# Performance work log

Measured on AMD Instinct MI355X. Metric: run time of the kernel, lower is better.

The kernel has to match this reference:

```python
import jax, jax.numpy as jnp
import numpy as np

B, C, W, H = 16, 512, 64, 64
OUT, NH = 512, 8
HD = OUT // NH          # 64
K = 64                  # kernel_size == attended axis length (height)


def setup_inputs() -> dict:
    key = jax.random.key(0)
    k0, k1, k2, k3 = jax.random.split(key, 4)
    s = float(HD) ** -0.5
    return {
        "x": jax.random.normal(k0, (B, C, W, H), jnp.float32),
        "in_proj_weight": jax.random.normal(k1, (2 * OUT, C), jnp.float32) * s,
        "in_proj_bias": jnp.zeros((2 * OUT,), jnp.float32),
        "out_proj_w": jax.random.normal(k2, (OUT, OUT), jnp.float32) * s,
        "out_proj_b": jnp.zeros((OUT,), jnp.float32),
        "relative": jax.random.normal(k3, (2 * HD, 2 * K - 1), jnp.float32) * s,
    }


def reference(x, in_proj_weight, in_proj_bias, out_proj_w, out_proj_b, relative):
    b, c, w, h = x.shape
    hd2 = HD // 2
    # width=False, self-attention path: permute(0,3,2,1) then flat view
    xq = jnp.transpose(x, (0, 3, 2, 1)).reshape(b * w, h, c)
    qkv = xq @ in_proj_weight.T + in_proj_bias
    q, k, v = jnp.split(qkv, [OUT // 2, OUT], axis=2)

    # relative position embeddings gathered into [2*HD, K, K]
    rel_idx = jnp.arange(K)[:, None] - jnp.arange(K)[None, :] + (K - 1)  # key i, query j
    emb = relative[:, rel_idx]                                          # [2*HD, K, K]
    q_emb, k_emb, v_emb = jnp.split(emb, [hd2, HD], axis=0)

    # [bw, heads, ch, pos]
    q = q.reshape(b * w, h, NH, hd2).transpose(0, 2, 3, 1)
    k = k.reshape(b * w, h, NH, hd2).transpose(0, 2, 3, 1)
    v = v.reshape(b * w, h, NH, HD).transpose(0, 2, 3, 1)

    qr = jnp.einsum('bgci,cij->bgij', q, q_emb)
    kr = jnp.einsum('bgci,cij->bgij', k, k_emb).swapaxes(2, 3)
    qk = jnp.einsum('bgci,bgcj->bgij', q, k)
    sim = jax.nn.softmax(qk + qr + kr, axis=3)

    sv = jnp.einsum('bgij,bgcj->bgci', sim, v)     # [bw, NH, HD, h]
    sve = jnp.einsum('bgij,cij->bgci', sim, v_emb)  # [bw, NH, HD, h]
    out = (sv + sve).reshape(b * w, OUT, h).swapaxes(1, 2)  # [bw, h, OUT]
    out = out @ out_proj_w.T + out_proj_b
    # [b, w, h, OUT] -> transpose(2,3) -> permute(0,2,3,1) == transpose(0,3,2,1)
    out = out.reshape(b, w, h, OUT).transpose(0, 3, 2, 1)   # [B, OUT, H, W]
    return out
```

## Files before the change

### kernel.cpp

```cpp
#include <hip/hip_runtime.h>

using u16 = unsigned short;
typedef __attribute__((ext_vector_type(8))) _Float16 h8v;
typedef __attribute__((ext_vector_type(8))) u16 us8;
typedef __attribute__((ext_vector_type(4))) float f4v;

__device__ __forceinline__ u16 f2h(float f) {
  _Float16 h = (_Float16)f;
  return __builtin_bit_cast(unsigned short, h);
}
__device__ __forceinline__ _Float16 bits2h(u16 u) {
  return __builtin_bit_cast(_Float16, u);
}

__device__ __forceinline__ f4v mfma16(h8v a, h8v b, f4v c) {
  return __builtin_amdgcn_mfma_f32_16x16x32_f16(a, b, c, 0, 0, 0);
}

__device__ __forceinline__ void gll16(const void* g, void* l) {
  __builtin_amdgcn_global_load_lds(
      (const __attribute__((address_space(1))) void*)g,
      (__attribute__((address_space(3))) void*)l, 16, 0, 0);
}


__global__ __launch_bounds__(256) void k0_setup(
    const float* __restrict__ w1, const float* __restrict__ wout,
    const float* __restrict__ rel, u16* __restrict__ W1b, u16* __restrict__ Woutb,
    u16* __restrict__ EqT, u16* __restrict__ EkT, u16* __restrict__ Evp)
{
  int idx = blockIdx.x * 256 + threadIdx.x;
  if (idx < 524288) {
    W1b[idx] = f2h(w1[idx]);
  } else if (idx < 786432) {
    int k = idx - 524288; Woutb[k] = f2h(wout[k]);
  } else if (idx < 790528) {
    int k = idx - 786432; int t = k >> 5, c = k & 31;
    EqT[k] = (t < 127) ? f2h(rel[c * 127 + t]) : (u16)0;
  } else if (idx < 794624) {
    int k = idx - 790528; int t = k >> 5, c = k & 31;
    EkT[k] = (t < 127) ? f2h(rel[(32 + c) * 127 + t]) : (u16)0;
  } else if (idx < 802816) {
    int k = idx - 794624; int c = k >> 7, t = k & 127;
    Evp[k] = (t < 127) ? f2h(rel[(64 + c) * 127 + t]) : (u16)0;
  }
}

__global__ __launch_bounds__(256) void k0t_transpose(
    const float* __restrict__ x, u16* __restrict__ xT)
{
  const int bid = blockIdx.x;
  const int cc = bid & 7, w = (bid >> 3) & 63, b = bid >> 9;
  const int c0 = cc * 64;
  const int t = threadIdx.x;
  __shared__ float T[64 * 65];

  const float* xb = x + ((size_t)(b * 512 + c0) * 64 + w) * 64;
#pragma unroll
  for (int p = 0; p < 4; p++) {
    int ci = (t >> 4) + p * 16;
    int pos = (t & 15) * 4;
    float4 v = *(const float4*)&xb[(size_t)ci * 4096 + pos];
    T[ci * 65 + pos + 0] = v.x; T[ci * 65 + pos + 1] = v.y;
    T[ci * 65 + pos + 2] = v.z; T[ci * 65 + pos + 3] = v.w;
  }
  __syncthreads();
  size_t Rb = (size_t)b * 4096 + (size_t)w * 64;
#pragma unroll
  for (int p = 0; p < 2; p++) {
    int u = p * 256 + t;
    int h = u >> 3, ch = u & 7;
    us8 o;
#pragma unroll
    for (int e = 0; e < 8; e++) o[e] = f2h(T[(ch * 8 + e) * 65 + h]);
    *(us8*)&xT[(Rb + h) * 512 + c0 + ch * 8] = o;
  }
}

__global__ __launch_bounds__(512, 1) void k1_qkv(
    const u16* __restrict__ xT, const u16* __restrict__ W1b,
    const float* __restrict__ bias, u16* __restrict__ qkv)
{
  __shared__ u16 POOL[81920];
  u16* XL = POOL;
  u16* Bl = POOL + 65536;
  const int rt = blockIdx.x;
  const int b = rt >> 5, w0 = (rt & 31) * 2;
  const int tid = threadIdx.x;
  const int l = tid & 63, wv = tid >> 6;
  const int lr = l & 15, lg = l >> 4;
  const int osub = (wv & 1) * 64;
  const int rsub = (wv >> 1) * 32;
  const size_t Rbase = (size_t)rt * 128;

#pragma unroll
  for (int i = 0; i < 16; i++) {
    int r = wv * 16 + i;
    gll16(xT + (Rbase + r) * 512 + ((l ^ (r & 7)) << 3), XL + r * 512);
  }

  auto stageB = [&](int ot, int kk, int buf) {
#pragma unroll
    for (int q = 0; q < 2; q++) {
      int slot = q * 512 + tid;
      int o = slot >> 3, c4 = slot & 7;
      gll16(W1b + (size_t)(ot * 128 + o) * 512 + kk * 64 + ((c4 ^ (o & 7)) << 3),
            Bl + buf * 8192 + slot * 8);
    }
  };

  stageB(0, 0, 0);
  __syncthreads();

  for (int ot = 0; ot < 8; ot++) {
    const int o0 = ot * 128;
    f4v acc[4][2];
#pragma unroll
    for (int mt = 0; mt < 4; mt++)
#pragma unroll
      for (int nt = 0; nt < 2; nt++) acc[mt][nt] = (f4v){0.f, 0.f, 0.f, 0.f};

#pragma unroll
    for (int kk = 0; kk < 8; kk++) {
      int cur = kk & 1;
      if (kk < 7) stageB(ot, kk + 1, cur ^ 1);
      h8v wf[4][2], xf[2][2];
#pragma unroll
      for (int mt = 0; mt < 4; mt++)
#pragma unroll
        for (int kc = 0; kc < 2; kc++) {
          int o = osub + mt * 16 + lr;
          wf[mt][kc] = *(const h8v*)&Bl[cur * 8192 + o * 64 +
                                        (((kc * 4 + lg) ^ (o & 7)) << 3)];
        }
#pragma unroll
      for (int nt = 0; nt < 2; nt++)
#pragma unroll
        for (int kc = 0; kc < 2; kc++) {
          int r = rsub + nt * 16 + lr;
          xf[nt][kc] = *(const h8v*)&XL[r * 512 + kk * 64 +
                                        (((kc * 4 + lg) ^ (r & 7)) << 3)];
        }
#pragma unroll
      for (int mt = 0; mt < 4; mt++)
#pragma unroll
        for (int nt = 0; nt < 2; nt++)
#pragma unroll
          for (int kc = 0; kc < 2; kc++)
            acc[mt][nt] = mfma16(wf[mt][kc], xf[nt][kc], acc[mt][nt]);
      __syncthreads();
    }

    u16* Tr = Bl;
#pragma unroll
    for (int mt = 0; mt < 4; mt++)
#pragma unroll
      for (int nt = 0; nt < 2; nt++) {
        int r = rsub + nt * 16 + lr;
#pragma unroll
        for (int ep = 0; ep < 2; ep++) {
          int o_ = osub + mt * 16 + lg * 4 + 2 * ep;
          float v0 = acc[mt][nt][2 * ep + 0] + bias[o0 + o_];
          float v1 = acc[mt][nt][2 * ep + 1] + bias[o0 + o_ + 1];
          unsigned pk = (unsigned)f2h(v0) | ((unsigned)f2h(v1) << 16);
          int cc = o_ >> 3;
          int dst = (cc & 8) | ((cc & 7) ^ (r & 7));
          *(unsigned*)&Tr[r * 128 + dst * 8 + (o_ & 7)] = pk;
        }
      }
    __syncthreads();
#pragma unroll
    for (int p = 0; p < 4; p++) {
      int u = p * 512 + tid;
      int r = u >> 4, cc = u & 15;
      int dst = (cc & 8) | ((cc & 7) ^ (r & 7));
      us8 v = *(const us8*)&Tr[r * 128 + dst * 8];
      int h = r & 63, wl = r >> 6;
      size_t S = (size_t)(b * 64 + h) * 64 + w0 + wl;
      *(us8*)&qkv[S * 1024 + o0 + cc * 8] = v;
    }
    __syncthreads();
    if (ot < 7) { stageB(ot + 1, 0, 0); __syncthreads(); }
  }
}

__global__ __launch_bounds__(256) void k2_attn(
    const u16* __restrict__ qkv, const u16* __restrict__ EqT,
    const u16* __restrict__ EkT, const u16* __restrict__ Evp,
    u16* __restrict__ attn)
{
  const int bid = blockIdx.x;
  const int s = bid >> 3, g = bid & 7;
  const int tid = threadIdx.x;
  const int l = tid & 63, wv = tid >> 6;
  const int lr = l & 15, lg = l >> 4;
  const int i0 = wv * 16;
  const u16* base = qkv + (size_t)s * 65536;

  __shared__ float QEt[128 * 68];
  __shared__ float KEt[64 * 128];
  u16* Pl  = (u16*)QEt;
  u16* VTl = (u16*)QEt + 4096;

  us8 vreg0, vreg1;
  {
    int u0 = tid,        j0_ = u0 >> 3, cb0 = u0 & 7;
    int u1 = tid + 256,  j1_ = u1 >> 3, cb1 = u1 & 7;
    vreg0 = *(const us8*)(base + j0_ * 1024 + 512 + g * 64 + cb0 * 8);
    vreg1 = *(const us8*)(base + j1_ * 1024 + 512 + g * 64 + cb1 * 8);
  }

  h8v qf = *(const h8v*)(base + (i0 + lr) * 1024 + g * 32 + lg * 8);
  h8v kf[4];
#pragma unroll
  for (int jt = 0; jt < 4; jt++)
    kf[jt] = *(const h8v*)(base + (jt * 16 + lr) * 1024 + 256 + g * 32 + lg * 8);

  const f4v z4 = {0.f, 0.f, 0.f, 0.f};

#pragma unroll
  for (int tt = 0; tt < 8; tt++) {
    h8v eb = *(const h8v*)(EqT + (tt * 16 + lr) * 32 + lg * 8);
    f4v d = mfma16(qf, eb, z4);
    *(f4v*)&QEt[(tt * 16 + lr) * 68 + i0 + lg * 4] = d;
  }
#pragma unroll
  for (int q = 0; q < 2; q++) {
    int tt = wv * 2 + q;
    h8v ea = *(const h8v*)(EkT + (tt * 16 + lr) * 32 + lg * 8);
#pragma unroll
    for (int jt = 0; jt < 4; jt++) {
      f4v d = mfma16(ea, kf[jt], z4);
      *(f4v*)&KEt[(jt * 16 + lr) * 128 + tt * 16 + lg * 4] = d;
    }
  }
  f4v sc[4];
#pragma unroll
  for (int jt = 0; jt < 4; jt++) sc[jt] = mfma16(qf, kf[jt], z4);

  __syncthreads();

  float pv[4][4];
#pragma unroll
  for (int jt = 0; jt < 4; jt++)
#pragma unroll
    for (int r = 0; r < 4; r++) {
      int i = i0 + lg * 4 + r;
      int j = jt * 16 + lr;
      int tq = i - j + 63;
      pv[jt][r] = sc[jt][r] + QEt[tq * 68 + i] + KEt[j * 128 + (126 - tq)];
    }
  float rsum[4];
#pragma unroll
  for (int r = 0; r < 4; r++) {
    float m = fmaxf(fmaxf(pv[0][r], pv[1][r]), fmaxf(pv[2][r], pv[3][r]));
    m = fmaxf(m, __shfl_xor(m, 1));
    m = fmaxf(m, __shfl_xor(m, 2));
    m = fmaxf(m, __shfl_xor(m, 4));
    m = fmaxf(m, __shfl_xor(m, 8));
    float t0 = 0.f;
#pragma unroll
    for (int jt = 0; jt < 4; jt++) {
      pv[jt][r] = exp2f((pv[jt][r] - m) * 1.4426950408889634f);
      t0 += pv[jt][r];
    }
    t0 += __shfl_xor(t0, 1);
    t0 += __shfl_xor(t0, 2);
    t0 += __shfl_xor(t0, 4);
    t0 += __shfl_xor(t0, 8);
    rsum[r] = t0;
  }

  __syncthreads();

#pragma unroll
  for (int jt = 0; jt < 4; jt++)
#pragma unroll
    for (int r = 0; r < 4; r++) {
      int i = i0 + lg * 4 + r;
      int j = jt * 16 + lr;
      Pl[i * 64 + (((j >> 3) ^ (i & 7)) << 3) + (j & 7)] = f2h(pv[jt][r]);
    }
  {
    int u0 = tid, j0_ = u0 >> 3, cb0 = u0 & 7;
#pragma unroll
    for (int e = 0; e < 8; e++) {
      int c = cb0 * 8 + e;
      VTl[c * 64 + (((j0_ >> 3) ^ (c & 7)) << 3) + (j0_ & 7)] = (u16)vreg0[e];
    }
    int u1 = tid + 256, j1_ = u1 >> 3, cb1 = u1 & 7;
#pragma unroll
    for (int e = 0; e < 8; e++) {
      int c = cb1 * 8 + e;
      VTl[c * 64 + (((j1_ >> 3) ^ (c & 7)) << 3) + (j1_ & 7)] = (u16)vreg1[e];
    }
  }
  __syncthreads();

  f4v acc[4] = {z4, z4, z4, z4};
  {
    int i = i0 + lr;
#pragma unroll
    for (int kc = 0; kc < 2; kc++) {
      h8v pa = *(const h8v*)&Pl[i * 64 + (((kc * 4 + lg) ^ (i & 7)) << 3)];
#pragma unroll
      for (int ct = 0; ct < 4; ct++) {
        int cA = ct * 16 + lr;
        h8v vb = *(const h8v*)&VTl[cA * 64 + (((kc * 4 + lg) ^ (cA & 7)) << 3)];
        acc[ct] = mfma16(pa, vb, acc[ct]);
      }
    }
#pragma unroll
    for (int tc = 0; tc < 4; tc++) {
      h8v pa;
#pragma unroll
      for (int e = 0; e < 8; e++) {
        int t = tc * 32 + lg * 8 + e;
        int j = i + 63 - t;
        int jc = j < 0 ? 0 : (j > 63 ? 63 : j);
        u16 tmp = Pl[i * 64 + (((jc >> 3) ^ (i & 7)) << 3) + (jc & 7)];
        pa[e] = (j >= 0 && j < 64) ? bits2h(tmp) : (_Float16)0.f;
      }
#pragma unroll
      for (int ct = 0; ct < 4; ct++) {
        h8v eb = *(const h8v*)(Evp + (ct * 16 + lr) * 128 + tc * 32 + lg * 8);
        acc[ct] = mfma16(pa, eb, acc[ct]);
      }
    }
  }
  float inv[4];
#pragma unroll
  for (int r = 0; r < 4; r++) inv[r] = 1.f / rsum[r];
#pragma unroll
  for (int ct = 0; ct < 4; ct++)
#pragma unroll
    for (int r = 0; r < 4; r++) {
      int i = i0 + lg * 4 + r;
      attn[(size_t)(s * 64 + i) * 512 + g * 64 + ct * 16 + lr] =
          f2h(acc[ct][r] * inv[r]);
    }
}

__global__ __launch_bounds__(512) void k3_oproj(
    const u16* __restrict__ attn, const u16* __restrict__ Woutb,
    const float* __restrict__ ob, float* __restrict__ out)
{
  const int bid = blockIdx.x;
  const int b = bid >> 6, w = bid & 63;
  const int tid = threadIdx.x;
  const int l = tid & 63, wv = tid >> 6;
  const int lr = l & 15, lg = l >> 4;

  __shared__ u16 Bl[2][64 * 64];

  f4v acc[4][4];
#pragma unroll
  for (int a_ = 0; a_ < 4; a_++)
#pragma unroll
    for (int b_ = 0; b_ < 4; b_++) acc[a_][b_] = (f4v){0.f, 0.f, 0.f, 0.f};

  auto stageB = [&](int kk, int buf) {
    int c0 = kk * 64;
    int h_l = wv * 8 + (l >> 3);
    int p = l & 7;
    const u16* src = attn + ((size_t)b * 4096 + (size_t)h_l * 64 + w) * 512 + c0 +
                     ((p ^ (h_l & 7)) << 3);
    gll16(src, &Bl[buf][wv * 512]);
  };

  stageB(0, 0);
  __syncthreads();

  for (int kk = 0; kk < 8; kk++) {
    int cur = kk & 1, nxt = cur ^ 1;
    if (kk < 7) stageB(kk + 1, nxt);
    int c0 = kk * 64;
    h8v af[4][2], bf[4][2];
#pragma unroll
    for (int mt = 0; mt < 4; mt++)
#pragma unroll
      for (int kc = 0; kc < 2; kc++)
        af[mt][kc] = *(const h8v*)(Woutb + (size_t)(wv * 64 + mt * 16 + lr) * 512 +
                                   c0 + kc * 32 + lg * 8);
#pragma unroll
    for (int jt = 0; jt < 4; jt++)
#pragma unroll
      for (int kc = 0; kc < 2; kc++) {
        int h = jt * 16 + lr;
        bf[jt][kc] = *(const h8v*)&Bl[cur][h * 64 + (((kc * 4 + lg) ^ (h & 7)) << 3)];
      }
#pragma unroll
    for (int mt = 0; mt < 4; mt++)
#pragma unroll
      for (int jt = 0; jt < 4; jt++)
#pragma unroll
        for (int kc = 0; kc < 2; kc++)
          acc[mt][jt] = mfma16(af[mt][kc], bf[jt][kc], acc[mt][jt]);
    __syncthreads();
  }

#pragma unroll
  for (int mt = 0; mt < 4; mt++)
#pragma unroll
    for (int jt = 0; jt < 4; jt++)
#pragma unroll
      for (int e = 0; e < 4; e++) {
        int o = wv * 64 + mt * 16 + lg * 4 + e;
        int h = jt * 16 + lr;
        out[(((size_t)b * 512 + o) * 64 + w) * 64 + h] = acc[mt][jt][e] + ob[o];
      }
}

extern "C" void kernel_launch(void* const* d_in, const int* in_sizes, int n_in,
                              void* d_out, int out_size, void* d_ws, size_t ws_size,
                              hipStream_t stream)
{
  (void)in_sizes; (void)n_in; (void)out_size; (void)ws_size;
  const float* x    = (const float*)d_in[0];
  const float* w1   = (const float*)d_in[1];
  const float* b1   = (const float*)d_in[2];
  const float* wout = (const float*)d_in[3];
  const float* bo   = (const float*)d_in[4];
  const float* rel  = (const float*)d_in[5];
  float* out = (float*)d_out;

  char* ws = (char*)d_ws;
  u16* qkv_ws  = (u16*)ws;
  u16* attn_ws = (u16*)(ws + 134217728);
  u16* xT_ws   = attn_ws;
  u16* W1b     = (u16*)(ws + 201326592);
  u16* Woutb   = (u16*)(ws + 202375168);
  u16* EqT     = (u16*)(ws + 202899456);
  u16* EkT     = (u16*)(ws + 202907648);
  u16* Evp     = (u16*)(ws + 202915840);

  k0_setup<<<dim3(3136), dim3(256), 0, stream>>>(w1, wout, rel, W1b, Woutb, EqT, EkT, Evp);
  k0t_transpose<<<dim3(8192), dim3(256), 0, stream>>>(x, xT_ws);
  k1_qkv  <<<dim3(512),  dim3(512), 0, stream>>>(xT_ws, W1b, b1, qkv_ws);
  k2_attn <<<dim3(8192), dim3(256), 0, stream>>>(qkv_ws, EqT, EkT, Evp, attn_ws);
  k3_oproj<<<dim3(1024), dim3(512), 0, stream>>>(attn_ws, Woutb, bo, out);
}
```

Before: 380.6 us.

## Shrink attention LDS to fp16 and prebuild shifted P for relative-V MFMA

Stores the relative query/key embedding logits in LDS as fp16 instead of fp32, with a transposed, padded KE layout, so shared memory per block shrinks. The launch bounds now ask for 4 blocks per CU. Softmax probabilities are also written into a diagonally shifted, zero-padded buffer. The relative-value MFMA operand then comes from one vector load instead of eight scalar gathered loads with bounds checks. The trade-offs are lower precision on the bias terms, extra LDS stores and a zero-fill pass, and possible register pressure from the occupancy hint.

Measured after the change: 344.0 us. 1.11x faster.

```diff
diff --git a/kernel.cpp b/kernel.cpp
--- a/kernel.cpp
+++ b/kernel.cpp
@@ -1,6 +1,7 @@
 #include <hip/hip_runtime.h>
 
 using u16 = unsigned short;
+using u32 = unsigned int;
 typedef __attribute__((ext_vector_type(8))) _Float16 h8v;
 typedef __attribute__((ext_vector_type(8))) u16 us8;
 typedef __attribute__((ext_vector_type(4))) float f4v;
@@ -184,7 +185,7 @@
   }
 }
 
-__global__ __launch_bounds__(256) void k2_attn(
+__global__ __launch_bounds__(256, 4) void k2_attn(
     const u16* __restrict__ qkv, const u16* __restrict__ EqT,
     const u16* __restrict__ EkT, const u16* __restrict__ Evp,
     u16* __restrict__ attn)
@@ -197,10 +198,12 @@
   const int i0 = wv * 16;
   const u16* base = qkv + (size_t)s * 65536;
 
-  __shared__ float QEt[128 * 68];
-  __shared__ float KEt[64 * 128];
-  u16* Pl  = (u16*)QEt;
-  u16* VTl = (u16*)QEt + 4096;
+  __shared__ __align__(16) u16 POOL[16896];
+  u16* QEt  = POOL;
+  u16* KEtT = POOL + 8448;
+  u16* Pl   = POOL;
+  u16* VTl  = POOL + 4096;
+  u16* Psh  = POOL + 8192;
 
   us8 vreg0, vreg1;
   {
@@ -222,7 +225,11 @@
   for (int tt = 0; tt < 8; tt++) {
     h8v eb = *(const h8v*)(EqT + (tt * 16 + lr) * 32 + lg * 8);
     f4v d = mfma16(qf, eb, z4);
-    *(f4v*)&QEt[(tt * 16 + lr) * 68 + i0 + lg * 4] = d;
+#pragma unroll
+    for (int p = 0; p < 2; p++) {
+      u32 pk = (u32)f2h(d[2 * p]) | ((u32)f2h(d[2 * p + 1]) << 16);
+      *(u32*)&QEt[(tt * 16 + lr) * 66 + i0 + lg * 4 + 2 * p] = pk;
+    }
   }
 #pragma unroll
   for (int q = 0; q < 2; q++) {
@@ -231,7 +238,9 @@
 #pragma unroll
     for (int jt = 0; jt < 4; jt++) {
       f4v d = mfma16(ea, kf[jt], z4);
-      *(f4v*)&KEt[(jt * 16 + lr) * 128 + tt * 16 + lg * 4] = d;
+#pragma unroll
+      for (int e = 0; e < 4; e++)
+        KEtT[(tt * 16 + 4 * lg + e) * 66 + jt * 16 + lr] = f2h(d[e]);
     }
   }
   f4v sc[4];
@@ -248,7 +257,8 @@
       int i = i0 + lg * 4 + r;
       int j = jt * 16 + lr;
       int tq = i - j + 63;
-      pv[jt][r] = sc[jt][r] + QEt[tq * 68 + i] + KEt[j * 128 + (126 - tq)];
+      pv[jt][r] = sc[jt][r] + (float)bits2h(QEt[tq * 66 + i]) +
+                  (float)bits2h(KEtT[(126 - tq) * 66 + j]);
     }
   float rsum[4];
 #pragma unroll
@@ -279,9 +289,21 @@
     for (int r = 0; r < 4; r++) {
       int i = i0 + lg * 4 + r;
       int j = jt * 16 + lr;
-      Pl[i * 64 + (((j >> 3) ^ (i & 7)) << 3) + (j & 7)] = f2h(pv[jt][r]);
+      u16 ph = f2h(pv[jt][r]);
+      Pl[i * 64 + (((j >> 3) ^ (i & 7)) << 3) + (j & 7)] = ph;
+      int d = i + 63 - j;
+      int cd = d >> 3;
+      Psh[i * 128 + (((cd & 8) | ((cd & 7) ^ (i & 7))) << 3) + (d & 7)] = ph;
     }
   {
+    int zi = tid >> 2;
+#pragma unroll
+    for (int kk = 0; kk < 16; kk++) {
+      int k = (tid & 3) * 16 + kk;
+      int col = (k < zi) ? k : (k + 64);
+      int cd = col >> 3;
+      Psh[zi * 128 + (((cd & 8) | ((cd & 7) ^ (zi & 7))) << 3) + (col & 7)] = 0;
+    }
     int u0 = tid, j0_ = u0 >> 3, cb0 = u0 & 7;
 #pragma unroll
     for (int e = 0; e < 8; e++) {
@@ -312,15 +334,9 @@
     }
 #pragma unroll
     for (int tc = 0; tc < 4; tc++) {
-      h8v pa;
-#pragma unroll
-      for (int e = 0; e < 8; e++) {
-        int t = tc * 32 + lg * 8 + e;
-        int j = i + 63 - t;
-        int jc = j < 0 ? 0 : (j > 63 ? 63 : j);
-        u16 tmp = Pl[i * 64 + (((jc >> 3) ^ (i & 7)) << 3) + (jc & 7)];
-        pa[e] = (j >= 0 && j < 64) ? bits2h(tmp) : (_Float16)0.f;
-      }
+      int cd = tc * 4 + lg;
+      int cds = (cd & 8) | ((cd & 7) ^ (i & 7));
+      h8v pa = *(const h8v*)&Psh[i * 128 + cds * 8];
 #pragma unroll
       for (int ct = 0; ct < 4; ct++) {
         h8v eb = *(const h8v*)(Evp + (ct * 16 + lr) * 128 + tc * 32 + lg * 8);
```
